# Performance work log

Hardware: AMD Instinct MI355X
Metric: run time of the kernel (lower is better)

The kernel has to match this reference:

```python
import jax, jax.numpy as jnp
import numpy as np

VOCAB = 50257
D = 1024
EDGES = [0, 20000, 40000, VOCAB]  # cluster boundaries
HSZ = [1024, 256, 64]             # D // 4**i per cluster


def setup_inputs() -> dict:
    key = jax.random.key(0)
    ks = jax.random.split(key, 8)
    emb_input = jax.random.randint(ks[0], (8, 2048), 0, VOCAB, dtype=jnp.int64)
    inp = {"emb_input": emb_input}
    for i in range(3):
        vsz = EDGES[i + 1] - EDGES[i]
        h = HSZ[i]
        inp[f"emb{i}"] = jax.random.normal(ks[1 + 2 * i], (vsz, h), dtype=jnp.float32) * 0.02
        # nn.Linear(h, D, bias=False) weight has shape [D, h]
        inp[f"w{i}"] = jax.random.normal(ks[2 + 2 * i], (D, h), dtype=jnp.float32) * 0.02
    return inp


def reference(emb_input, emb0, w0, emb1, w1, emb2, w2):
    B, S = emb_input.shape
    idx = emb_input.reshape(-1)  # [N]
    clusters = [(emb0, w0), (emb1, w1), (emb2, w2)]
    out = jnp.zeros((idx.shape[0], D), dtype=jnp.float32)
    for i, (emb, w) in enumerate(clusters):
        lo, hi = EDGES[i], EDGES[i + 1]
        mask = (idx >= lo) & (idx < hi)                       # [N]
        local = jnp.clip(idx - lo, 0, emb.shape[0] - 1)       # in-range gather ids
        h = emb[local]                                        # [N, hsz_i]
        proj = jnp.einsum('nh,dh->nd', h, w)                  # [N, D]
        out = out + jnp.where(mask[:, None], proj, 0.0)
    return out.reshape(B, S, D)
```

## Files before the change

### kernel.cpp

```cpp
#include <hip/hip_runtime.h>
#include <hip/hip_bf16.h>
#include <stdint.h>

#define DOUT 1024
#define NMAX 16384

typedef __attribute__((ext_vector_type(8))) short short8;
typedef __attribute__((ext_vector_type(4))) float floatx4;

__device__ __forceinline__ unsigned short f2bf(float f) {
  union { float f; uint32_t u; } v;
  v.f = f;
  return (unsigned short)((v.u + 0x7FFFu + ((v.u >> 16) & 1u)) >> 16);
}

__device__ __forceinline__ short8 cvt8(float4 a, float4 b) {
  __hip_bfloat162 p0 = __float22bfloat162_rn(make_float2(a.x, a.y));
  __hip_bfloat162 p1 = __float22bfloat162_rn(make_float2(a.z, a.w));
  __hip_bfloat162 p2 = __float22bfloat162_rn(make_float2(b.x, b.y));
  __hip_bfloat162 p3 = __float22bfloat162_rn(make_float2(b.z, b.w));
  union { __hip_bfloat162 h[4]; short8 s; } u;
  u.h[0] = p0; u.h[1] = p1; u.h[2] = p2; u.h[3] = p3;
  return u.s;
}

__global__ __launch_bounds__(256) void classify_cvt_kernel(
    const int* __restrict__ idx, int* __restrict__ cnt,
    int* __restrict__ bucket, int* __restrict__ blocal, int N,
    const float* __restrict__ w0, const float* __restrict__ w1,
    const float* __restrict__ w2, unsigned short* __restrict__ wb0,
    unsigned short* __restrict__ wb1, unsigned short* __restrict__ wb2) {
  if (blockIdx.x < 64) {
    int n = blockIdx.x * 256 + threadIdx.x;
    int lane = threadIdx.x & 63;
    int c = -1, v = 0;
    if (n < N) {
      v = idx[n];
      c = (v < 20000) ? 0 : ((v < 40000) ? 1 : 2);
    }
#pragma unroll
    for (int k = 0; k < 3; ++k) {
      unsigned long long m = __ballot(c == k);
      if (c == k) {
        int leader = __ffsll((unsigned long long)m) - 1;
        int base = 0;
        if (lane == leader) base = atomicAdd(&cnt[k], (int)__popcll(m));
        base = __shfl(base, leader);
        int rank = (int)__popcll(m & ((1ull << (unsigned)lane) - 1ull));
        int lo = (k == 0) ? 0 : (k == 1) ? 20000 : 40000;
        bucket[k * NMAX + base + rank] = n;
        blocal[k * NMAX + base + rank] = v - lo;
      }
    }
  } else {
    int i = (blockIdx.x - 64) * 256 + threadIdx.x;
    if (i >= 344064) return;
    const float4* src;
    ushort4* dst;
    if (i < 262144) {
      src = (const float4*)w0 + i;
      dst = (ushort4*)wb0 + i;
    } else if (i < 327680) {
      src = (const float4*)w1 + (i - 262144);
      dst = (ushort4*)wb1 + (i - 262144);
    } else {
      src = (const float4*)w2 + (i - 327680);
      dst = (ushort4*)wb2 + (i - 327680);
    }
    float4 v = *src;
    ushort4 o;
    o.x = f2bf(v.x); o.y = f2bf(v.y); o.z = f2bf(v.z); o.w = f2bf(v.w);
    *dst = o;
  }
}

__global__ __launch_bounds__(256) void gather_kernel(
    const float* __restrict__ emb0, const float* __restrict__ emb1,
    const float* __restrict__ emb2, const int* __restrict__ cnt,
    const int* __restrict__ blocal, unsigned short* __restrict__ Abf) {
  const int b = blockIdx.x;
  const int c0 = cnt[0], c1 = cnt[1], c2 = cnt[2];
  const float* emb;
  const int* bl;
  int H, count, baseRow, lg;
  size_t off;
  if (b < 4096) {
    emb = emb0; bl = blocal; H = 1024; count = c0; off = 0;
    baseRow = b * 4; lg = 6;
  } else if (b < 5120) {
    emb = emb1; bl = blocal + NMAX; H = 256; count = c1;
    off = (size_t)c0 * 1024; baseRow = (b - 4096) * 16; lg = 4;
  } else {
    emb = emb2; bl = blocal + 2 * NMAX; H = 64; count = c2;
    off = (size_t)c0 * 1024 + (size_t)c1 * 256; baseRow = (b - 5120) * 64; lg = 2;
  }
  const int tid = threadIdx.x;
  const int r = baseRow + (tid >> lg);
  if (r >= count) return;
  const int e = (tid & ((1 << lg) - 1)) * 16;
  const float* src = emb + (size_t)bl[r] * H + e;
  unsigned short* d = Abf + off + (size_t)r * H + e;
  float4 v0 = ((const float4*)src)[0];
  float4 v1 = ((const float4*)src)[1];
  float4 v2 = ((const float4*)src)[2];
  float4 v3 = ((const float4*)src)[3];
  *(short8*)d = cvt8(v0, v1);
  *(short8*)(d + 8) = cvt8(v2, v3);
}

template <int H>
__device__ __forceinline__ void gemm_body(
    const unsigned short* __restrict__ A, const unsigned short* __restrict__ B,
    int count, const int* __restrict__ bucket, float* __restrict__ out,
    unsigned short* As, unsigned short* Bs, int* rowTok) {
  const int m0 = blockIdx.y * 128;
  if (m0 >= count) return;
  const int n0 = blockIdx.x * 128;

  const int tid = threadIdx.x;
  const int wave = tid >> 6;
  const int lane = tid & 63;
  const int quad = lane >> 4;
  const int l16 = lane & 15;
  const int wm = wave & 1;
  const int wn = wave >> 1;

  if (tid < 128) {
    int m = m0 + tid;
    rowTok[tid] = (m < count) ? bucket[m] : -1;
  }

  floatx4 acc[4][4];
#pragma unroll
  for (int i = 0; i < 4; ++i)
#pragma unroll
    for (int j = 0; j < 4; ++j) acc[i][j] = (floatx4){0.f, 0.f, 0.f, 0.f};

  const char* Ab = (const char*)A;
  const char* Bb = (const char*)B;
  const int row = tid >> 2;
  const int ck = tid & 3;

  for (int k0 = 0; k0 < H; k0 += 64) {
    __syncthreads();
#pragma unroll
    for (int t = 0; t < 2; ++t)
#pragma unroll
      for (int p = 0; p < 2; ++p) {
        const void* ga =
            Ab + ((size_t)(m0 + p * 64 + row) * H + k0 + t * 32) * 2 + ck * 16;
        void* la = (char*)As + (t * 8192 + p * 4096 + wave * 1024);
        __builtin_amdgcn_global_load_lds(
            (const __attribute__((address_space(1))) void*)ga,
            (__attribute__((address_space(3))) void*)la, 16, 0, 0);
        const void* gb =
            Bb + ((size_t)(n0 + p * 64 + row) * H + k0 + t * 32) * 2 + ck * 16;
        void* lb = (char*)Bs + (t * 8192 + p * 4096 + wave * 1024);
        __builtin_amdgcn_global_load_lds(
            (const __attribute__((address_space(1))) void*)gb,
            (__attribute__((address_space(3))) void*)lb, 16, 0, 0);
      }
    __syncthreads();

#pragma unroll
    for (int t = 0; t < 2; ++t) {
      short8 af[4], bf[4];
#pragma unroll
      for (int mi = 0; mi < 4; ++mi)
        af[mi] = *(const short8*)&As[t * 4096 + (wm * 64 + mi * 16 + l16) * 32 + quad * 8];
#pragma unroll
      for (int ni = 0; ni < 4; ++ni)
        bf[ni] = *(const short8*)&Bs[t * 4096 + (wn * 64 + ni * 16 + l16) * 32 + quad * 8];
#pragma unroll
      for (int mi = 0; mi < 4; ++mi)
#pragma unroll
        for (int ni = 0; ni < 4; ++ni)
          acc[mi][ni] = __builtin_amdgcn_mfma_f32_16x16x32_bf16(
              af[mi], bf[ni], acc[mi][ni], 0, 0, 0);
    }
  }

  const int colBase = n0 + wn * 64 + l16;
#pragma unroll
  for (int mi = 0; mi < 4; ++mi) {
#pragma unroll
    for (int r = 0; r < 4; ++r) {
      int tok = rowTok[wm * 64 + mi * 16 + quad * 4 + r];
      if (tok >= 0) {
        float* o = out + (size_t)tok * DOUT + colBase;
#pragma unroll
        for (int ni = 0; ni < 4; ++ni) o[ni * 16] = acc[mi][ni][r];
      }
    }
  }
}

__global__ __launch_bounds__(256) void gemm_bucketed(
    const unsigned short* __restrict__ Abf,
    const unsigned short* __restrict__ wb0,
    const unsigned short* __restrict__ wb1,
    const unsigned short* __restrict__ wb2, const int* __restrict__ cnt,
    const int* __restrict__ bucket, float* __restrict__ out) {
  __shared__ __align__(16) unsigned short As[2 * 128 * 32];
  __shared__ __align__(16) unsigned short Bs[2 * 128 * 32];
  __shared__ int rowTok[128];

  const int z = blockIdx.z;
  const int c0 = cnt[0];
  const int c1 = cnt[1];
  if (z == 0)
    gemm_body<1024>(Abf, wb0, c0, bucket, out, As, Bs, rowTok);
  else if (z == 1)
    gemm_body<256>(Abf + (size_t)c0 * 1024, wb1, c1, bucket + NMAX, out, As,
                   Bs, rowTok);
  else
    gemm_body<64>(Abf + (size_t)c0 * 1024 + (size_t)c1 * 256, wb2, cnt[2],
                  bucket + 2 * NMAX, out, As, Bs, rowTok);
}

extern "C" void kernel_launch(void* const* d_in, const int* in_sizes, int n_in,
                              void* d_out, int out_size, void* d_ws, size_t ws_size,
                              hipStream_t stream) {
  const int* idx = (const int*)d_in[0];
  const float* emb0 = (const float*)d_in[1];
  const float* w0 = (const float*)d_in[2];
  const float* emb1 = (const float*)d_in[3];
  const float* w1 = (const float*)d_in[4];
  const float* emb2 = (const float*)d_in[5];
  const float* w2 = (const float*)d_in[6];
  float* out = (float*)d_out;
  const int N = in_sizes[0];

  char* ws = (char*)d_ws;
  int* cnt = (int*)ws;
  int* bucket = (int*)(ws + 1024);
  int* blocal = bucket + 3 * NMAX;
  size_t off = 1024 + (size_t)6 * NMAX * 4;
  off = (off + 255) & ~(size_t)255;
  unsigned short* wb0 = (unsigned short*)(ws + off); off += (size_t)DOUT * 1024 * 2;
  unsigned short* wb1 = (unsigned short*)(ws + off); off += (size_t)DOUT * 256 * 2;
  unsigned short* wb2 = (unsigned short*)(ws + off); off += (size_t)DOUT * 64 * 2;
  off = (off + 255) & ~(size_t)255;
  unsigned short* Abf = (unsigned short*)(ws + off);
  off += (size_t)(NMAX + 128) * 1024 * 2;

  hipMemsetAsync(cnt, 0, 16 * sizeof(int), stream);

  classify_cvt_kernel<<<64 + 1344, 256, 0, stream>>>(
      idx, cnt, bucket, blocal, N, w0, w1, w2, wb0, wb1, wb2);

  gather_kernel<<<5376, 256, 0, stream>>>(emb0, emb1, emb2, cnt, blocal, Abf);

  dim3 grid(DOUT / 128, NMAX / 128, 3);
  gemm_bucketed<<<grid, 256, 0, stream>>>(Abf, wb0, wb1, wb2, cnt, bucket, out);
}
```

Measured before the change: 198.4 us.

## Rewrite bucketed GEMM with 256x128 tiles, triple-buffered LDS pipeline, swizzle

```diff
diff --git a/kernel.cpp b/kernel.cpp
--- a/kernel.cpp
+++ b/kernel.cpp
@@ -4,6 +4,11 @@
 
 #define DOUT 1024
 #define NMAX 16384
+
+#define BM 256
+#define BN 128
+#define LDSBUF 49152
+#define BOFFS 32768
 
 typedef __attribute__((ext_vector_type(8))) short short8;
 typedef __attribute__((ext_vector_type(4))) float floatx4;
@@ -112,72 +117,112 @@
 __device__ __forceinline__ void gemm_body(
     const unsigned short* __restrict__ A, const unsigned short* __restrict__ B,
     int count, const int* __restrict__ bucket, float* __restrict__ out,
-    unsigned short* As, unsigned short* Bs, int* rowTok) {
-  const int m0 = blockIdx.y * 128;
+    char* lds, int* rowTok) {
+  const int m0 = blockIdx.y * BM;
   if (m0 >= count) return;
-  const int n0 = blockIdx.x * 128;
+  const int n0 = blockIdx.x * BN;
+  constexpr int NT = H / 64;
 
   const int tid = threadIdx.x;
   const int wave = tid >> 6;
   const int lane = tid & 63;
   const int quad = lane >> 4;
   const int l16 = lane & 15;
-  const int wm = wave & 1;
-  const int wn = wave >> 1;
-
-  if (tid < 128) {
+  const int wm = wave & 3;
+  const int wn = wave >> 2;
+
+  if (tid < BM) {
     int m = m0 + tid;
     rowTok[tid] = (m < count) ? bucket[m] : -1;
   }
 
+  const int dl = wave * 1024 + lane * 16;
+  const int lswz = dl ^ (((dl >> 7) & 3) << 4);
+  const int rW = lswz >> 6;
+  const int ckW = (lswz >> 4) & 3;
+  const char* Abyte = (const char*)A;
+  const char* Bbyte = (const char*)B;
+  const size_t aOff0 = ((size_t)(m0 + rW) * H) * 2 + ckW * 16;
+  const size_t aOff1 = ((size_t)(m0 + 128 + rW) * H) * 2 + ckW * 16;
+  const size_t bOff = ((size_t)(n0 + rW) * H) * 2 + ckW * 16;
+
+  auto stage = [&](int kt, char* buf) {
+    const int kb = kt * 128;
+#pragma unroll
+    for (int s = 0; s < 2; ++s) {
+      __builtin_amdgcn_global_load_lds(
+          (const __attribute__((address_space(1))) void*)(Abyte + aOff0 + kb + s * 64),
+          (__attribute__((address_space(3))) void*)(buf + s * 16384 + wave * 1024),
+          16, 0, 0);
+      __builtin_amdgcn_global_load_lds(
+          (const __attribute__((address_space(1))) void*)(Abyte + aOff1 + kb + s * 64),
+          (__attribute__((address_space(3))) void*)(buf + s * 16384 + 8192 + wave * 1024),
+          16, 0, 0);
+      __builtin_amdgcn_global_load_lds(
+          (const __attribute__((address_space(1))) void*)(Bbyte + bOff + kb + s * 64),
+          (__attribute__((address_space(3))) void*)(buf + BOFFS + s * 8192 + wave * 1024),
+          16, 0, 0);
+    }
+  };
+
+  int offA[2][4], offB[2][4];
+#pragma unroll
+  for (int s = 0; s < 2; ++s) {
+#pragma unroll
+    for (int i = 0; i < 4; ++i) {
+      int ba = (wm * 64 + i * 16 + l16) * 64 + quad * 16;
+      offA[s][i] = s * 16384 + (ba ^ (((ba >> 7) & 3) << 4));
+      int bb = (wn * 64 + i * 16 + l16) * 64 + quad * 16;
+      offB[s][i] = BOFFS + s * 8192 + (bb ^ (((bb >> 7) & 3) << 4));
+    }
+  }
+
+  if (NT >= 1) stage(0, lds);
+  if (NT >= 2) stage(1, lds + LDSBUF);
+  if (NT >= 3) stage(2, lds + 2 * LDSBUF);
+
   floatx4 acc[4][4];
 #pragma unroll
   for (int i = 0; i < 4; ++i)
 #pragma unroll
     for (int j = 0; j < 4; ++j) acc[i][j] = (floatx4){0.f, 0.f, 0.f, 0.f};
 
-  const char* Ab = (const char*)A;
-  const char* Bb = (const char*)B;
-  const int row = tid >> 2;
-  const int ck = tid & 3;
-
-  for (int k0 = 0; k0 < H; k0 += 64) {
-    __syncthreads();
-#pragma unroll
-    for (int t = 0; t < 2; ++t)
-#pragma unroll
-      for (int p = 0; p < 2; ++p) {
-        const void* ga =
-            Ab + ((size_t)(m0 + p * 64 + row) * H + k0 + t * 32) * 2 + ck * 16;
-        void* la = (char*)As + (t * 8192 + p * 4096 + wave * 1024);
-        __builtin_amdgcn_global_load_lds(
-            (const __attribute__((address_space(1))) void*)ga,
-            (__attribute__((address_space(3))) void*)la, 16, 0, 0);
-        const void* gb =
-            Bb + ((size_t)(n0 + p * 64 + row) * H + k0 + t * 32) * 2 + ck * 16;
-        void* lb = (char*)Bs + (t * 8192 + p * 4096 + wave * 1024);
-        __builtin_amdgcn_global_load_lds(
-            (const __attribute__((address_space(1))) void*)gb,
-            (__attribute__((address_space(3))) void*)lb, 16, 0, 0);
-      }
-    __syncthreads();
-
-#pragma unroll
-    for (int t = 0; t < 2; ++t) {
-      short8 af[4], bf[4];
-#pragma unroll
-      for (int mi = 0; mi < 4; ++mi)
-        af[mi] = *(const short8*)&As[t * 4096 + (wm * 64 + mi * 16 + l16) * 32 + quad * 8];
-#pragma unroll
-      for (int ni = 0; ni < 4; ++ni)
-        bf[ni] = *(const short8*)&Bs[t * 4096 + (wn * 64 + ni * 16 + l16) * 32 + quad * 8];
-#pragma unroll
-      for (int mi = 0; mi < 4; ++mi)
-#pragma unroll
-        for (int ni = 0; ni < 4; ++ni)
-          acc[mi][ni] = __builtin_amdgcn_mfma_f32_16x16x32_bf16(
-              af[mi], bf[ni], acc[mi][ni], 0, 0, 0);
-    }
+#pragma unroll
+  for (int kt = 0; kt < NT; ++kt) {
+    const int rem = NT - 1 - kt;
+    if (rem >= 2)
+      asm volatile("s_waitcnt vmcnt(12)" ::: "memory");
+    else if (rem == 1)
+      asm volatile("s_waitcnt vmcnt(6)" ::: "memory");
+    else
+      asm volatile("s_waitcnt vmcnt(0)" ::: "memory");
+    asm volatile("s_barrier" ::: "memory");
+
+    const char* buf = lds + (kt % 3) * LDSBUF;
+#pragma unroll
+    for (int ph = 0; ph < 4; ++ph) {
+      const int mh = ph >> 1, nh = ph & 1;
+      short8 a[2][2], b[2][2];
+#pragma unroll
+      for (int s = 0; s < 2; ++s)
+#pragma unroll
+        for (int i = 0; i < 2; ++i) {
+          a[s][i] = *(const short8*)(buf + offA[s][mh * 2 + i]);
+          b[s][i] = *(const short8*)(buf + offB[s][nh * 2 + i]);
+        }
+      __builtin_amdgcn_s_setprio(1);
+#pragma unroll
+      for (int s = 0; s < 2; ++s)
+#pragma unroll
+        for (int i = 0; i < 2; ++i)
+#pragma unroll
+          for (int j = 0; j < 2; ++j)
+            acc[mh * 2 + i][nh * 2 + j] = __builtin_amdgcn_mfma_f32_16x16x32_bf16(
+                a[s][i], b[s][j], acc[mh * 2 + i][nh * 2 + j], 0, 0, 0);
+      __builtin_amdgcn_s_setprio(0);
+    }
+    asm volatile("s_barrier" ::: "memory");
+    if (kt + 3 < NT) stage(kt + 3, lds + (kt % 3) * LDSBUF);
   }
 
   const int colBase = n0 + wn * 64 + l16;
@@ -195,27 +240,26 @@
   }
 }
 
-__global__ __launch_bounds__(256) void gemm_bucketed(
+__global__ __launch_bounds__(512, 2) void gemm_pipe(
     const unsigned short* __restrict__ Abf,
     const unsigned short* __restrict__ wb0,
     const unsigned short* __restrict__ wb1,
     const unsigned short* __restrict__ wb2, const int* __restrict__ cnt,
     const int* __restrict__ bucket, float* __restrict__ out) {
-  __shared__ __align__(16) unsigned short As[2 * 128 * 32];
-  __shared__ __align__(16) unsigned short Bs[2 * 128 * 32];
-  __shared__ int rowTok[128];
+  __shared__ __align__(16) char lds[3 * LDSBUF + BM * 4];
+  int* rowTok = (int*)(lds + 3 * LDSBUF);
 
   const int z = blockIdx.z;
   const int c0 = cnt[0];
   const int c1 = cnt[1];
   if (z == 0)
-    gemm_body<1024>(Abf, wb0, c0, bucket, out, As, Bs, rowTok);
+    gemm_body<1024>(Abf, wb0, c0, bucket, out, lds, rowTok);
   else if (z == 1)
-    gemm_body<256>(Abf + (size_t)c0 * 1024, wb1, c1, bucket + NMAX, out, As,
-                   Bs, rowTok);
+    gemm_body<256>(Abf + (size_t)c0 * 1024, wb1, c1, bucket + NMAX, out, lds,
+                   rowTok);
   else
     gemm_body<64>(Abf + (size_t)c0 * 1024 + (size_t)c1 * 256, wb2, cnt[2],
-                  bucket + 2 * NMAX, out, As, Bs, rowTok);
+                  bucket + 2 * NMAX, out, lds, rowTok);
 }
 
 extern "C" void kernel_launch(void* const* d_in, const int* in_sizes, int n_in,
@@ -242,7 +286,7 @@
   unsigned short* wb2 = (unsigned short*)(ws + off); off += (size_t)DOUT * 64 * 2;
   off = (off + 255) & ~(size_t)255;
   unsigned short* Abf = (unsigned short*)(ws + off);
-  off += (size_t)(NMAX + 128) * 1024 * 2;
+  off += (size_t)(NMAX + 256) * 1024 * 2;
 
   hipMemsetAsync(cnt, 0, 16 * sizeof(int), stream);
 
@@ -251,6 +295,6 @@
 
   gather_kernel<<<5376, 256, 0, stream>>>(emb0, emb1, emb2, cnt, blocal, Abf);
 
-  dim3 grid(DOUT / 128, NMAX / 128, 3);
-  gemm_bucketed<<<grid, 256, 0, stream>>>(Abf, wb0, wb1, wb2, cnt, bucket, out);
-}
+  dim3 grid(DOUT / BN, NMAX / BM, 3);
+  gemm_pipe<<<grid, 512, 0, stream>>>(Abf, wb0, wb1, wb2, cnt, bucket, out);
+}
```

Measured after the change: 197.7 us. Within noise of the previous version (-0.3%).
